# Optimization experiments

Hardware: AMD Instinct MI355X
Metric: run time of the kernel (lower is better)

Reference implementation:

```python
import jax, jax.numpy as jnp
import numpy as np

LAYERS = 3
N_NODES = 100000
N_EDGES = 800000
EMB = 100
EPS = 1e-12  # F.normalize default eps


def setup_inputs() -> dict:
    key = jax.random.key(0)
    ks = jax.random.split(key, 7)
    embedding = jax.random.normal(ks[0], (N_NODES, EMB), dtype=jnp.float32)
    adj_val = jax.random.uniform(ks[1], (N_EDGES,), dtype=jnp.float32)
    w_att = jax.random.normal(ks[2], (EMB, 1), dtype=jnp.float32) * 0.1
    b_att = jax.random.normal(ks[3], (1,), dtype=jnp.float32) * 0.1
    w_items = jax.random.normal(ks[4], (LAYERS, EMB, EMB), dtype=jnp.float32) * 0.1
    adj_row = jax.random.randint(ks[5], (N_EDGES,), 0, N_NODES, dtype=jnp.int32)
    adj_col = jax.random.randint(ks[6], (N_EDGES,), 0, N_NODES, dtype=jnp.int32)
    return {"embedding": embedding, "adj_val": adj_val, "w_att": w_att,
            "b_att": b_att, "w_items": w_items, "adj_row": adj_row, "adj_col": adj_col}


def reference(embedding, adj_val, w_att, b_att, w_items, adj_row, adj_col):
    n = embedding.shape[0]
    # column-degree normalization: adjacency.multiply(1/adjacency.sum(axis=0))
    degree = jax.ops.segment_sum(adj_val, adj_col, num_segments=n)  # [N]
    vals = adj_val / degree[adj_col]  # per-edge normalized value

    x = embedding
    final = embedding
    for i in range(LAYERS):
        scores = x @ w_att + b_att              # [N,1]
        attw = jax.nn.softmax(scores, axis=0)   # softmax over nodes (dim=0)
        x = x @ w_items[i].T                    # nn.Linear (no bias)
        m = x * attw                            # attention-weighted features
        # sparse mm: out[r] = sum_{edges e: row[e]=r} vals[e] * m[col[e]]
        gathered = m[adj_col] * vals[:, None]   # [E, EMB]
        x = jax.ops.segment_sum(gathered, adj_row, num_segments=n)
        # F.normalize(p=2, dim=-1)
        norm = jnp.linalg.norm(x, axis=-1, keepdims=True)
        x = x / jnp.maximum(norm, EPS)
        final = final + x
    return final / (LAYERS + 1)
```

## Files before the change

### kernel.cpp

```cpp
#include <hip/hip_runtime.h>
#include <hip/hip_bf16.h>

#define NN 100000
#define NE 800000
#define EM 100
#define NL 3

typedef short bf16x8 __attribute__((ext_vector_type(8)));
typedef float f32x4  __attribute__((ext_vector_type(4)));

static constexpr size_t OFF_XB   = 0;
static constexpr size_t OFF_M    = OFF_XB   + (size_t)NN*128*2;
static constexpr size_t OFF_F    = OFF_M    + (size_t)NN*EM*2;
static constexpr size_t OFF_DEG  = OFF_F    + (size_t)NN*EM*2;
static constexpr size_t OFF_SC   = OFF_DEG  + (size_t)NN*4;
static constexpr size_t OFF_ES   = OFF_SC   + (size_t)NN*4;
static constexpr size_t OFF_CNT  = OFF_ES   + (size_t)NE*8;
static constexpr size_t OFF_RP   = OFF_CNT  + (size_t)NN*4;
static constexpr size_t OFF_CUR  = OFF_RP   + (size_t)(NN+64)*4;
static constexpr size_t OFF_BS   = OFF_CUR  + (size_t)NN*4;
static constexpr size_t OFF_RED  = OFF_BS   + 512;
static constexpr size_t OFF_FLAG = OFF_RED  + 64;
static constexpr size_t OFF_WAT  = OFF_FLAG + 16;
static constexpr size_t OFF_WBF  = OFF_WAT  + 512;

__device__ inline float ldf(const void* p, int i, int f32) {
    return f32 ? ((const float*)p)[i]
               : __bfloat162float(((const __hip_bfloat16*)p)[i]);
}

__device__ inline float bflo(unsigned int u) { return __uint_as_float(u << 16); }
__device__ inline float bfhi(unsigned int u) { return __uint_as_float(u & 0xFFFF0000u); }
__device__ inline unsigned int pack2bf(float a, float b) {
    __hip_bfloat16 ha = __float2bfloat16(a), hb = __float2bfloat16(b);
    unsigned short ua = *(unsigned short*)&ha, ub = *(unsigned short*)&hb;
    return (unsigned int)ua | ((unsigned int)ub << 16);
}

__device__ inline int probe_block(const void* p, int nsamp) {
    __shared__ int sflag;
    int tid = threadIdx.x;
    if (tid < 64) {
        const unsigned short* h = (const unsigned short*)p;
        int big = 0;
        for (int i = tid; i < nsamp; i += 64) {
            int ex = (h[2 * i] >> 7) & 0xFF;
            big += (ex >= 134) ? 1 : 0;
        }
        #pragma unroll
        for (int off = 32; off; off >>= 1) big += __shfl_xor(big, off);
        if (tid == 0) sflag = (big >= 2) ? 1 : 0;
    }
    __syncthreads();
    int f = sflag;
    __syncthreads();
    return f;
}

__global__ __launch_bounds__(256) void k_setup(const void* w_att, const void* w_itm,
                                               float* deg, int* counts, float* red,
                                               float* wat, unsigned short* wbf) {
    int fw = probe_block(w_att, 50);
    int fi = probe_block(w_itm, 256);
    int i = blockIdx.x * 256 + threadIdx.x;
    if (i < NN) { deg[i] = 0.f; counts[i] = 0; }
    if (i < 8)  red[i] = 0.f;
    if (i < EM) wat[i] = ldf(w_att, i, fw);
    if (i < NL * 112 * 128) {
        int l = i / (112 * 128), rem = i % (112 * 128);
        int n = rem >> 7, k = rem & 127;
        float v = (n < EM && k < EM) ? ldf(w_itm, (l * EM + n) * EM + k, fi) : 0.f;
        __hip_bfloat16 b = __float2bfloat16(v);
        wbf[i] = *(unsigned short*)&b;
    }
}

__global__ __launch_bounds__(256) void k_initxf(const void* __restrict__ emb,
                                                const float* __restrict__ wat,
                                                unsigned int* __restrict__ xbf,
                                                unsigned int* __restrict__ fin,
                                                float* __restrict__ scores, int* flags) {
    int femb = probe_block(emb, 256);
    if (blockIdx.x == 0 && threadIdx.x == 0) flags[0] = femb;
    int lane = threadIdx.x & 63, w = threadIdx.x >> 6;
    int r = blockIdx.x * 4 + w;
    if (r >= NN) return;
    float f0 = 0.f, f1 = 0.f, part = 0.f;
    bool act = lane < 50;
    if (act) {
        if (femb) {
            float2 t = ((const float2*)emb)[(size_t)r * 50 + lane];
            f0 = t.x; f1 = t.y;
        } else {
            unsigned int u = ((const unsigned int*)emb)[(size_t)r * 50 + lane];
            f0 = bflo(u); f1 = bfhi(u);
        }
        float2 wv = *(const float2*)(wat + 2 * lane);
        part = f0 * wv.x + f1 * wv.y;
        fin[(size_t)r * 50 + lane] = pack2bf(f0, f1);
    }
    xbf[(size_t)r * 64 + lane] = act ? pack2bf(f0, f1) : 0u;
    #pragma unroll
    for (int off = 32; off; off >>= 1) part += __shfl_xor(part, off);
    if (lane == 0) scores[r] = part;
}

__global__ __launch_bounds__(256) void k_deg(const void* __restrict__ val,
                                             const int* __restrict__ row, const int* __restrict__ col,
                                             float* deg, int* counts) {
    int fav = probe_block(val, 256);
    int e = blockIdx.x * 256 + threadIdx.x;
    if (e >= NE) return;
    atomicAdd(&deg[col[e]], ldf(val, e, fav));
    atomicAdd(&counts[row[e]], 1);
}

__global__ __launch_bounds__(256) void k_scanA(const int* __restrict__ counts, int* excl, int* bsum) {
    __shared__ int s[256];
    int base = blockIdx.x * 1024;
    int tid = threadIdx.x;
    int v[4]; int t = 0;
    #pragma unroll
    for (int i = 0; i < 4; i++) {
        int idx = base + tid * 4 + i;
        v[i] = (idx < NN) ? counts[idx] : 0;
        t += v[i];
    }
    s[tid] = t; __syncthreads();
    for (int off = 1; off < 256; off <<= 1) {
        int add = (tid >= off) ? s[tid - off] : 0;
        __syncthreads();
        s[tid] += add;
        __syncthreads();
    }
    int ex = (tid == 0) ? 0 : s[tid - 1];
    #pragma unroll
    for (int i = 0; i < 4; i++) {
        int idx = base + tid * 4 + i;
        if (idx < NN) excl[idx] = ex;
        ex += v[i];
    }
    if (tid == 255) bsum[blockIdx.x] = s[255];
}

__global__ __launch_bounds__(256) void k_scanC(int* rowptr, int* cursor, const int* __restrict__ bsum) {
    __shared__ int spfx;
    int tid = threadIdx.x;
    int gi = blockIdx.x >> 2;
    if (tid < 64) {
        int t = (tid < gi) ? bsum[tid] : 0;
        if (tid + 64 < gi) t += bsum[tid + 64];
        #pragma unroll
        for (int off = 32; off; off >>= 1) t += __shfl_xor(t, off);
        if (tid == 0) spfx = t;
    }
    __syncthreads();
    int pfx = spfx;
    int i = blockIdx.x * 256 + tid;
    if (i < NN) {
        int v = rowptr[i] + pfx;
        rowptr[i] = v; cursor[i] = v;
        if (i == 0) rowptr[NN] = NE;
    }
}

__global__ __launch_bounds__(256) void k_scatter(const int* __restrict__ row, const int* __restrict__ col,
                                                 const void* __restrict__ aval,
                                                 const float* __restrict__ deg, int* cursor,
                                                 int2* es) {
    int fav = probe_block(aval, 256);
    int e = blockIdx.x * 256 + threadIdx.x;
    if (e >= NE) return;
    int r = row[e];
    int c = col[e];
    int pos = atomicAdd(&cursor[r], 1);
    float v = ldf(aval, e, fav) / deg[c];
    es[pos] = make_int2(c, __float_as_int(v));
}

__global__ __launch_bounds__(256) void k_expsum(float* __restrict__ scores, float* red, int layer) {
    __shared__ float ss[4];
    int n = blockIdx.x * 256 + threadIdx.x;
    float p = 0.f;
    if (n < NN) { p = expf(scores[n]); scores[n] = p; }
    float t = p;
    #pragma unroll
    for (int off = 32; off; off >>= 1) t += __shfl_xor(t, off);
    if ((threadIdx.x & 63) == 0) ss[threadIdx.x >> 6] = t;
    __syncthreads();
    if (threadIdx.x == 0) atomicAdd(&red[2 * layer + 1], ss[0] + ss[1] + ss[2] + ss[3]);
}

__global__ __launch_bounds__(256) void k_gemm(const unsigned short* __restrict__ xbf,
                                              const unsigned short* __restrict__ wbf,
                                              const float* __restrict__ scores,
                                              const float* __restrict__ red,
                                              unsigned short* __restrict__ m, int layer) {
    int wid = threadIdx.x >> 6, lane = threadIdx.x & 63;
    int row0 = blockIdx.x * 64 + wid * 16;
    if (row0 >= NN) return;
    int c15 = lane & 15, quad = lane >> 4;
    float inv_sum = 1.0f / red[2 * layer + 1];

    const bf16x8* xa = (const bf16x8*)(xbf + (size_t)(row0 + c15) * 128 + quad * 8);
    bf16x8 a[4];
    #pragma unroll
    for (int kq = 0; kq < 4; kq++) a[kq] = xa[kq * 4];

    float att[4];
    #pragma unroll
    for (int r = 0; r < 4; r++) att[r] = scores[row0 + quad * 4 + r] * inv_sum;

    const bf16x8* wb = (const bf16x8*)(wbf + (size_t)layer * 112 * 128
                                       + (size_t)c15 * 128 + quad * 8);
    #pragma unroll
    for (int nt = 0; nt < 7; nt++) {
        f32x4 acc = {0.f, 0.f, 0.f, 0.f};
        #pragma unroll
        for (int kq = 0; kq < 4; kq++) {
            bf16x8 b = wb[nt * 256 + kq * 4];
            acc = __builtin_amdgcn_mfma_f32_16x16x32_bf16(a[kq], b, acc, 0, 0, 0);
        }
        int col = nt * 16 + c15;
        if (col < EM) {
            #pragma unroll
            for (int r = 0; r < 4; r++) {
                int grow = row0 + quad * 4 + r;
                __hip_bfloat16 bv = __float2bfloat16(acc[r] * att[r]);
                m[(size_t)grow * EM + col] = *(unsigned short*)&bv;
            }
        }
    }
}

__global__ __launch_bounds__(256) void k_spmm(const int* __restrict__ rowptr,
                                              const int2* __restrict__ es,
                                              const unsigned short* __restrict__ m,
                                              const float* __restrict__ wat,
                                              unsigned int* __restrict__ xbf,
                                              unsigned int* __restrict__ fin,
                                              float* __restrict__ scores,
                                              void* __restrict__ out, const int* flags, int last) {
    int lane = threadIdx.x & 63;
    int w = threadIdx.x >> 6;
    int r = blockIdx.x * 4 + w;
    if (r >= NN) return;
    int s = rowptr[r], e = rowptr[r + 1];
    bool act = lane < 50;
    float a0 = 0.f, a1 = 0.f, b0 = 0.f, b1 = 0.f;
    for (int i = s; i < e; i += 8) {
        int2 cv[8];
        cv[0] = es[i];
        #pragma unroll
        for (int j = 1; j < 8; j++)
            cv[j] = (i + j < e) ? es[i + j] : make_int2(cv[0].x, 0);
        unsigned int u[8] = {0u, 0u, 0u, 0u, 0u, 0u, 0u, 0u};
        if (act) {
            #pragma unroll
            for (int j = 0; j < 8; j++)
                u[j] = *(const unsigned int*)(m + (size_t)cv[j].x * EM + 2 * lane);
        }
        #pragma unroll
        for (int j = 0; j < 8; j += 2) {
            float va = __int_as_float(cv[j].y), vb = __int_as_float(cv[j + 1].y);
            a0 += va * bflo(u[j]);     a1 += va * bfhi(u[j]);
            b0 += vb * bflo(u[j + 1]); b1 += vb * bfhi(u[j + 1]);
        }
    }
    a0 += b0; a1 += b1;
    float sq = a0 * a0 + a1 * a1;
    #pragma unroll
    for (int off = 32; off; off >>= 1) sq += __shfl_xor(sq, off);
    float rn = 1.f / fmaxf(sqrtf(sq), 1e-12f);
    float n0 = a0 * rn, n1 = a1 * rn;

    float part = 0.f;
    if (!last) xbf[(size_t)r * 64 + lane] = pack2bf(n0, n1);
    if (act) {
        size_t pidx = (size_t)r * 50 + lane;
        unsigned int fu = fin[pidx];
        float fn0 = bflo(fu) + n0, fn1 = bfhi(fu) + n1;
        if (!last) {
            fin[pidx] = pack2bf(fn0, fn1);
            float2 wv = *(const float2*)(wat + 2 * lane);
            part = n0 * wv.x + n1 * wv.y;
        } else {
            float o0 = fn0 * 0.25f, o1 = fn1 * 0.25f;
            if (flags[0]) ((float2*)out)[pidx] = make_float2(o0, o1);
            else          ((unsigned int*)out)[pidx] = pack2bf(o0, o1);
        }
    }
    if (!last) {
        #pragma unroll
        for (int off = 32; off; off >>= 1) part += __shfl_xor(part, off);
        if (lane == 0) scores[r] = part;
    }
}

extern "C" void kernel_launch(void* const* d_in, const int* in_sizes, int n_in,
                              void* d_out, int out_size, void* d_ws, size_t ws_size,
                              hipStream_t stream) {
    const void* emb   = d_in[0];
    const void* aval  = d_in[1];
    const void* w_att = d_in[2];
    const void* w_itm = d_in[4];
    const int* arow = (const int*)d_in[5];
    const int* acol = (const int*)d_in[6];

    char* w = (char*)d_ws;
    unsigned int*   xbf    = (unsigned int*)(w + OFF_XB);
    unsigned short* m      = (unsigned short*)(w + OFF_M);
    unsigned int*   fin    = (unsigned int*)(w + OFF_F);
    float*          deg    = (float*)(w + OFF_DEG);
    float*          scores = (float*)(w + OFF_SC);
    int2*           es     = (int2*) (w + OFF_ES);
    int*            counts = (int*)  (w + OFF_CNT);
    int*            rowptr = (int*)  (w + OFF_RP);
    int*            cursor = (int*)  (w + OFF_CUR);
    int*            bsum   = (int*)  (w + OFF_BS);
    float*          red    = (float*)(w + OFF_RED);
    int*            flags  = (int*)  (w + OFF_FLAG);
    float*          wat    = (float*)(w + OFF_WAT);
    unsigned short* wbf    = (unsigned short*)(w + OFF_WBF);

    const int GN   = (NN + 255) / 256;
    const int GNE  = (NE + 255) / 256;
    const int GSCN = (NN + 1023) / 1024;
    const int GW4  = (NN + 3) / 4;
    const int GGE  = (NN + 63) / 64;

    k_setup<<<GN, 256, 0, stream>>>(w_att, w_itm, deg, counts, red, wat, wbf);
    k_initxf<<<GW4, 256, 0, stream>>>(emb, wat, xbf, fin, scores, flags);
    k_deg<<<GNE, 256, 0, stream>>>(aval, arow, acol, deg, counts);
    k_scanA<<<GSCN, 256, 0, stream>>>(counts, rowptr, bsum);
    k_scanC<<<GN, 256, 0, stream>>>(rowptr, cursor, bsum);
    k_scatter<<<GNE, 256, 0, stream>>>(arow, acol, aval, deg, cursor, es);

    for (int l = 0; l < NL; l++) {
        k_expsum<<<GN, 256, 0, stream>>>(scores, red, l);
        k_gemm<<<GGE, 256, 0, stream>>>((const unsigned short*)xbf, wbf, scores, red, m, l);
        k_spmm<<<GW4, 256, 0, stream>>>(rowptr, es, m, wat, xbf, fin, scores,
                                        d_out, flags, (l == NL - 1) ? 1 : 0);
    }
}
```

Before: 585.0 us.

## Quantize message matrix to int8 with per-row scale and fuse softmax sum

Stores the attention-weighted message rows as int8 with a per-row float scale packed into 128-byte rows, so the edge gather in the sparse aggregation reads fewer bytes. The exponentiation and softmax denominator are now produced by the kernels that compute scores, accumulated into 256 atomic bins, which removes the separate exp-sum kernel per layer. This trades accuracy (8-bit quantization of intermediate features) for reduced memory traffic and fewer launches.

```diff
diff --git a/kernel.cpp b/kernel.cpp
--- a/kernel.cpp
+++ b/kernel.cpp
@@ -11,7 +11,7 @@
 
 static constexpr size_t OFF_XB   = 0;
 static constexpr size_t OFF_M    = OFF_XB   + (size_t)NN*128*2;
-static constexpr size_t OFF_F    = OFF_M    + (size_t)NN*EM*2;
+static constexpr size_t OFF_F    = OFF_M    + (size_t)NN*128;
 static constexpr size_t OFF_DEG  = OFF_F    + (size_t)NN*EM*2;
 static constexpr size_t OFF_SC   = OFF_DEG  + (size_t)NN*4;
 static constexpr size_t OFF_ES   = OFF_SC   + (size_t)NN*4;
@@ -19,8 +19,8 @@
 static constexpr size_t OFF_RP   = OFF_CNT  + (size_t)NN*4;
 static constexpr size_t OFF_CUR  = OFF_RP   + (size_t)(NN+64)*4;
 static constexpr size_t OFF_BS   = OFF_CUR  + (size_t)NN*4;
-static constexpr size_t OFF_RED  = OFF_BS   + 512;
-static constexpr size_t OFF_FLAG = OFF_RED  + 64;
+static constexpr size_t OFF_BIN  = OFF_BS   + 512;
+static constexpr size_t OFF_FLAG = OFF_BIN  + 4096;
 static constexpr size_t OFF_WAT  = OFF_FLAG + 16;
 static constexpr size_t OFF_WBF  = OFF_WAT  + 512;
 
@@ -58,13 +58,13 @@
 }
 
 __global__ __launch_bounds__(256) void k_setup(const void* w_att, const void* w_itm,
-                                               float* deg, int* counts, float* red,
+                                               float* deg, int* counts, float* bins,
                                                float* wat, unsigned short* wbf) {
     int fw = probe_block(w_att, 50);
     int fi = probe_block(w_itm, 256);
     int i = blockIdx.x * 256 + threadIdx.x;
     if (i < NN) { deg[i] = 0.f; counts[i] = 0; }
-    if (i < 8)  red[i] = 0.f;
+    if (i < 1024) bins[i] = 0.f;
     if (i < EM) wat[i] = ldf(w_att, i, fw);
     if (i < NL * 112 * 128) {
         int l = i / (112 * 128), rem = i % (112 * 128);
@@ -79,7 +79,8 @@
                                                 const float* __restrict__ wat,
                                                 unsigned int* __restrict__ xbf,
                                                 unsigned int* __restrict__ fin,
-                                                float* __restrict__ scores, int* flags) {
+                                                float* __restrict__ scores, int* flags,
+                                                float* __restrict__ bins) {
     int femb = probe_block(emb, 256);
     if (blockIdx.x == 0 && threadIdx.x == 0) flags[0] = femb;
     int lane = threadIdx.x & 63, w = threadIdx.x >> 6;
@@ -102,7 +103,11 @@
     xbf[(size_t)r * 64 + lane] = act ? pack2bf(f0, f1) : 0u;
     #pragma unroll
     for (int off = 32; off; off >>= 1) part += __shfl_xor(part, off);
-    if (lane == 0) scores[r] = part;
+    if (lane == 0) {
+        float p = expf(part);
+        scores[r] = p;
+        atomicAdd(&bins[r & 255], p);
+    }
 }
 
 __global__ __launch_bounds__(256) void k_deg(const void* __restrict__ val,
@@ -178,29 +183,21 @@
     es[pos] = make_int2(c, __float_as_int(v));
 }
 
-__global__ __launch_bounds__(256) void k_expsum(float* __restrict__ scores, float* red, int layer) {
-    __shared__ float ss[4];
-    int n = blockIdx.x * 256 + threadIdx.x;
-    float p = 0.f;
-    if (n < NN) { p = expf(scores[n]); scores[n] = p; }
-    float t = p;
-    #pragma unroll
-    for (int off = 32; off; off >>= 1) t += __shfl_xor(t, off);
-    if ((threadIdx.x & 63) == 0) ss[threadIdx.x >> 6] = t;
-    __syncthreads();
-    if (threadIdx.x == 0) atomicAdd(&red[2 * layer + 1], ss[0] + ss[1] + ss[2] + ss[3]);
-}
-
 __global__ __launch_bounds__(256) void k_gemm(const unsigned short* __restrict__ xbf,
                                               const unsigned short* __restrict__ wbf,
                                               const float* __restrict__ scores,
-                                              const float* __restrict__ red,
-                                              unsigned short* __restrict__ m, int layer) {
+                                              const float* __restrict__ bins,
+                                              signed char* __restrict__ m2, int layer) {
     int wid = threadIdx.x >> 6, lane = threadIdx.x & 63;
     int row0 = blockIdx.x * 64 + wid * 16;
     if (row0 >= NN) return;
     int c15 = lane & 15, quad = lane >> 4;
-    float inv_sum = 1.0f / red[2 * layer + 1];
+
+    f32x4 bv = ((const f32x4*)(bins + layer * 256))[lane];
+    float bsum = bv[0] + bv[1] + bv[2] + bv[3];
+    #pragma unroll
+    for (int off = 32; off; off >>= 1) bsum += __shfl_xor(bsum, off);
+    float inv_sum = 1.0f / bsum;
 
     const bf16x8* xa = (const bf16x8*)(xbf + (size_t)(row0 + c15) * 128 + quad * 8);
     bf16x8 a[4];
@@ -213,6 +210,7 @@
 
     const bf16x8* wb = (const bf16x8*)(wbf + (size_t)layer * 112 * 128
                                        + (size_t)c15 * 128 + quad * 8);
+    f32x4 accs[7];
     #pragma unroll
     for (int nt = 0; nt < 7; nt++) {
         f32x4 acc = {0.f, 0.f, 0.f, 0.f};
@@ -221,13 +219,25 @@
             bf16x8 b = wb[nt * 256 + kq * 4];
             acc = __builtin_amdgcn_mfma_f32_16x16x32_bf16(a[kq], b, acc, 0, 0, 0);
         }
-        int col = nt * 16 + c15;
-        if (col < EM) {
-            #pragma unroll
-            for (int r = 0; r < 4; r++) {
-                int grow = row0 + quad * 4 + r;
-                __hip_bfloat16 bv = __float2bfloat16(acc[r] * att[r]);
-                m[(size_t)grow * EM + col] = *(unsigned short*)&bv;
+        accs[nt] = acc;
+    }
+    #pragma unroll
+    for (int r = 0; r < 4; r++) {
+        float mx = 0.f;
+        #pragma unroll
+        for (int nt = 0; nt < 7; nt++) mx = fmaxf(mx, fabsf(accs[nt][r]));
+        #pragma unroll
+        for (int off = 1; off < 16; off <<= 1) mx = fmaxf(mx, __shfl_xor(mx, off));
+        float inv = 127.0f / fmaxf(mx, 1e-30f);
+        int grow = row0 + quad * 4 + r;
+        if (c15 == 0)
+            *(float*)(m2 + (size_t)grow * 128) = att[r] * mx * (1.0f / 127.0f);
+        #pragma unroll
+        for (int nt = 0; nt < 7; nt++) {
+            int col = nt * 16 + c15;
+            if (col < EM) {
+                int q = (int)rintf(accs[nt][r] * inv);
+                m2[(size_t)grow * 128 + 4 + col] = (signed char)q;
             }
         }
     }
@@ -235,12 +245,14 @@
 
 __global__ __launch_bounds__(256) void k_spmm(const int* __restrict__ rowptr,
                                               const int2* __restrict__ es,
-                                              const unsigned short* __restrict__ m,
+                                              const signed char* __restrict__ m2,
                                               const float* __restrict__ wat,
                                               unsigned int* __restrict__ xbf,
                                               unsigned int* __restrict__ fin,
                                               float* __restrict__ scores,
-                                              void* __restrict__ out, const int* flags, int last) {
+                                              void* __restrict__ out, const int* flags,
+                                              float* __restrict__ bins,
+                                              int layer, int last) {
     int lane = threadIdx.x & 63;
     int w = threadIdx.x >> 6;
     int r = blockIdx.x * 4 + w;
@@ -254,17 +266,25 @@
         #pragma unroll
         for (int j = 1; j < 8; j++)
             cv[j] = (i + j < e) ? es[i + j] : make_int2(cv[0].x, 0);
+        float t[8];
+        #pragma unroll
+        for (int j = 0; j < 8; j++) {
+            int cu = __builtin_amdgcn_readfirstlane(cv[j].x);
+            float sc = *(const float*)(m2 + (size_t)cu * 128);
+            t[j] = __int_as_float(cv[j].y) * sc;
+        }
         unsigned int u[8] = {0u, 0u, 0u, 0u, 0u, 0u, 0u, 0u};
         if (act) {
             #pragma unroll
             for (int j = 0; j < 8; j++)
-                u[j] = *(const unsigned int*)(m + (size_t)cv[j].x * EM + 2 * lane);
+                u[j] = *(const unsigned short*)(m2 + (size_t)cv[j].x * 128 + 4 + 2 * lane);
         }
         #pragma unroll
         for (int j = 0; j < 8; j += 2) {
-            float va = __int_as_float(cv[j].y), vb = __int_as_float(cv[j + 1].y);
-            a0 += va * bflo(u[j]);     a1 += va * bfhi(u[j]);
-            b0 += vb * bflo(u[j + 1]); b1 += vb * bfhi(u[j + 1]);
+            a0 += t[j]     * (float)(int)(signed char)(u[j] & 0xFF);
+            a1 += t[j]     * (float)(int)(signed char)(u[j] >> 8);
+            b0 += t[j + 1] * (float)(int)(signed char)(u[j + 1] & 0xFF);
+            b1 += t[j + 1] * (float)(int)(signed char)(u[j + 1] >> 8);
         }
     }
     a0 += b0; a1 += b1;
@@ -293,7 +313,11 @@
     if (!last) {
         #pragma unroll
         for (int off = 32; off; off >>= 1) part += __shfl_xor(part, off);
-        if (lane == 0) scores[r] = part;
+        if (lane == 0) {
+            float p = expf(part);
+            scores[r] = p;
+            atomicAdd(&bins[(layer + 1) * 256 + (r & 255)], p);
+        }
     }
 }
 
@@ -309,7 +333,7 @@
 
     char* w = (char*)d_ws;
     unsigned int*   xbf    = (unsigned int*)(w + OFF_XB);
-    unsigned short* m      = (unsigned short*)(w + OFF_M);
+    signed char*    m2     = (signed char*)(w + OFF_M);
     unsigned int*   fin    = (unsigned int*)(w + OFF_F);
     float*          deg    = (float*)(w + OFF_DEG);
     float*          scores = (float*)(w + OFF_SC);
@@ -318,7 +342,7 @@
     int*            rowptr = (int*)  (w + OFF_RP);
     int*            cursor = (int*)  (w + OFF_CUR);
     int*            bsum   = (int*)  (w + OFF_BS);
-    float*          red    = (float*)(w + OFF_RED);
+    float*          bins   = (float*)(w + OFF_BIN);
     int*            flags  = (int*)  (w + OFF_FLAG);
     float*          wat    = (float*)(w + OFF_WAT);
     unsigned short* wbf    = (unsigned short*)(w + OFF_WBF);
@@ -329,17 +353,16 @@
     const int GW4  = (NN + 3) / 4;
     const int GGE  = (NN + 63) / 64;
 
-    k_setup<<<GN, 256, 0, stream>>>(w_att, w_itm, deg, counts, red, wat, wbf);
-    k_initxf<<<GW4, 256, 0, stream>>>(emb, wat, xbf, fin, scores, flags);
+    k_setup<<<GN, 256, 0, stream>>>(w_att, w_itm, deg, counts, bins, wat, wbf);
+    k_initxf<<<GW4, 256, 0, stream>>>(emb, wat, xbf, fin, scores, flags, bins);
     k_deg<<<GNE, 256, 0, stream>>>(aval, arow, acol, deg, counts);
     k_scanA<<<GSCN, 256, 0, stream>>>(counts, rowptr, bsum);
     k_scanC<<<GN, 256, 0, stream>>>(rowptr, cursor, bsum);
     k_scatter<<<GNE, 256, 0, stream>>>(arow, acol, aval, deg, cursor, es);
 
     for (int l = 0; l < NL; l++) {
-        k_expsum<<<GN, 256, 0, stream>>>(scores, red, l);
-        k_gemm<<<GGE, 256, 0, stream>>>((const unsigned short*)xbf, wbf, scores, red, m, l);
-        k_spmm<<<GW4, 256, 0, stream>>>(rowptr, es, m, wat, xbf, fin, scores,
-                                        d_out, flags, (l == NL - 1) ? 1 : 0);
-    }
-}
+        k_gemm<<<GGE, 256, 0, stream>>>((const unsigned short*)xbf, wbf, scores, bins, m2, l);
+        k_spmm<<<GW4, 256, 0, stream>>>(rowptr, es, m2, wat, xbf, fin, scores,
+                                        d_out, flags, bins, l, (l == NL - 1) ? 1 : 0);
+    }
+}
```

Result: slower. 845.7 us (+44.6%).
